# Kernel optimization log

Hardware: AMD Instinct MI355X
Metric: run time of the kernel (lower is better)

Reference implementation:

```python
import jax, jax.numpy as jnp
import numpy as np

CH_IN = 256
CH_OUT = 32


def setup_inputs() -> dict:
    key = jax.random.key(0)
    ks = jax.random.split(key, 7)
    b, c, H, W = 4, CH_IN, 64, 64
    x = jax.random.normal(ks[0], (b, c, H, W), dtype=jnp.float32)
    # 1x1 conv weights (out, in) and biases, small init like torch default
    sc_in = 1.0 / np.sqrt(CH_IN)
    Wf = jax.random.uniform(ks[1], (CH_OUT, CH_IN), jnp.float32, -sc_in, sc_in)
    bf = jax.random.uniform(ks[2], (CH_OUT,), jnp.float32, -sc_in, sc_in)
    Wg = jax.random.uniform(ks[3], (CH_OUT, CH_IN), jnp.float32, -sc_in, sc_in)
    bg = jax.random.uniform(ks[4], (CH_OUT,), jnp.float32, -sc_in, sc_in)
    Wh = jax.random.uniform(ks[5], (CH_IN, CH_IN), jnp.float32, -sc_in, sc_in)
    bh = jax.random.uniform(ks[6], (CH_IN,), jnp.float32, -sc_in, sc_in)
    return {"x": x, "Wf": Wf, "bf": bf, "Wg": Wg, "bg": bg, "Wh": Wh, "bh": bh}


def reference(x, Wf, bf, Wg, bg, Wh, bh):
    b, c, H, W = x.shape
    xf = x.reshape(b, c, H * W)                      # [b, c, N]
    # 1x1 convs == per-pixel linear projections
    f = jnp.einsum('oc,bcn->bon', Wf, xf) + bf[None, :, None]   # [b, ch_out, N]
    g = jnp.einsum('oc,bcn->bon', Wg, xf) + bg[None, :, None]   # [b, ch_out, N]
    h = jnp.einsum('oc,bcn->bon', Wh, xf) + bh[None, :, None]   # [b, ch_in, N]
    # s[b, i, j] = sum_o f[b,o,i] * g[b,o,j]
    s = jnp.einsum('boi,boj->bij', f, g)             # [b, N, N]
    # torch softmax over dim=1 (the i axis)
    beta = jax.nn.softmax(s, axis=1)                 # [b, N, N]
    # o = h @ beta : [b, c, N] x [b, N, N] -> [b, c, N]
    o = jnp.einsum('bcn,bnm->bcm', h, beta)
    return o.reshape(b, c, H, W)
```

## Files before the change

### kernel.cpp

```cpp
#include <hip/hip_runtime.h>
#include <hip/hip_bf16.h>
#include <math.h>

#define BATCH 4
#define CIN   256
#define DQK   32
#define NPIX  4096
#define MTOT  320

typedef __attribute__((ext_vector_type(4))) float f32x4;
typedef __attribute__((ext_vector_type(8))) short bf16x8;
typedef __attribute__((ext_vector_type(4))) unsigned int u32x4;

__device__ __forceinline__ unsigned short f2bf(float f) {
  unsigned u = __builtin_bit_cast(unsigned, f);
  u += 0x7FFFu + ((u >> 16) & 1u);
  return (unsigned short)(u >> 16);
}
__device__ __forceinline__ unsigned pk2(float a, float b) {
  return (unsigned)f2bf(a) | ((unsigned)f2bf(b) << 16);
}
__device__ __forceinline__ void wait_vm2_lgkm0() { asm volatile("s_waitcnt vmcnt(2) lgkmcnt(0)" ::: "memory"); }
__device__ __forceinline__ void wait_vm0_lgkm0() { asm volatile("s_waitcnt vmcnt(0) lgkmcnt(0)" ::: "memory"); }

#define GLD16(GP, LP) \
  __builtin_amdgcn_global_load_lds((const __attribute__((address_space(1))) void*)(GP), \
                                   (__attribute__((address_space(3))) void*)(LP), 16, 0, 0)

__global__ void wcvt(const float* __restrict__ Wh, const float* __restrict__ Wf,
                     const float* __restrict__ Wg,
                     const float* __restrict__ bh, const float* __restrict__ bf,
                     const float* __restrict__ bg,
                     unsigned short* __restrict__ Wb, float* __restrict__ bcat) {
  const int r = blockIdx.x;
  const int c = threadIdx.x;
  const float* src = (r < 256) ? &Wh[r * CIN] : (r < 288) ? &Wf[(r - 256) * CIN] : &Wg[(r - 288) * CIN];
  Wb[r * CIN + c] = f2bf(src[c]);
  if (c == 0)
    bcat[r] = (r < 256) ? bh[r] : (r < 288) ? bf[r - 256] : bg[r - 288];
}

#define XPAD 4
__launch_bounds__(512, 1)
__global__ void proj_all(const float* __restrict__ x, const unsigned short* __restrict__ Wb,
                         const float* __restrict__ bcat,
                         unsigned short* __restrict__ F, unsigned short* __restrict__ G,
                         unsigned short* __restrict__ H) {
  __shared__ unsigned short Xs[64 * (CIN + XPAD)];

  const int bid = blockIdx.x;
  const int b = bid >> 6;
  const int n0 = (bid & 63) << 6;
  const int t = threadIdx.x;
  const int lane = t & 63;
  const int w = t >> 6;

  const float* __restrict__ xb = x + (size_t)b * CIN * NPIX + n0;
#pragma unroll
  for (int p = 0; p < 16; ++p) {
    const int k = p * 16 + w * 2;
    const float a0 = xb[(size_t)k * NPIX + lane];
    const float a1 = xb[(size_t)(k + 1) * NPIX + lane];
    const unsigned pk = (unsigned)f2bf(a0) | ((unsigned)f2bf(a1) << 16);
    *(unsigned*)((char*)Xs + lane * (CIN + XPAD) * 2 + k * 2) = pk;
  }
  __syncthreads();

  const int l16 = lane & 15, lhi = lane >> 4;
  const int wm = w >> 1;
  const int wn = w & 1;

  const f32x4 fzero = {0.f, 0.f, 0.f, 0.f};
  f32x4 acc[5][2];
#pragma unroll
  for (int i = 0; i < 5; ++i)
#pragma unroll
    for (int j = 0; j < 2; ++j) acc[i][j] = fzero;

#pragma unroll
  for (int ks = 0; ks < 8; ++ks) {
    bf16x8 bx[2];
#pragma unroll
    for (int j = 0; j < 2; ++j)
      bx[j] = *(const bf16x8*)&Xs[(wn * 32 + j * 16 + l16) * (CIN + XPAD) + ks * 32 + lhi * 8];
#pragma unroll
    for (int i = 0; i < 5; ++i) {
      const bf16x8 aw = *(const bf16x8*)(Wb + (size_t)(wm * 80 + i * 16 + l16) * CIN + ks * 32 + lhi * 8);
#pragma unroll
      for (int j = 0; j < 2; ++j)
        acc[i][j] = __builtin_amdgcn_mfma_f32_16x16x32_bf16(aw, bx[j], acc[i][j], 0, 0, 0);
    }
  }

#pragma unroll
  for (int i = 0; i < 5; ++i) {
    const int MT = wm * 5 + i;
    const int m0 = MT * 16;
    const f32x4 bias = *(const f32x4*)&bcat[m0 + lhi * 4];
#pragma unroll
    for (int j = 0; j < 2; ++j) {
      const int n = n0 + wn * 32 + j * 16 + l16;
      f32x4 v = acc[i][j];
      v.x += bias.x; v.y += bias.y; v.z += bias.z; v.w += bias.w;
      if (MT < 16) {
        const int c0 = m0 + lhi * 4;
        unsigned short* dst = H + ((size_t)b * CIN + c0) * NPIX + n;
        dst[0 * NPIX] = f2bf(v.x);
        dst[1 * NPIX] = f2bf(v.y);
        dst[2 * NPIX] = f2bf(v.z);
        dst[3 * NPIX] = f2bf(v.w);
      } else {
        unsigned short* dst = (MT < 18) ? F : G;
        const int d0 = ((MT - 16) & 1) * 16 + lhi * 4;
        uint2 pk;
        pk.x = (unsigned)f2bf(v.x) | ((unsigned)f2bf(v.y) << 16);
        pk.y = (unsigned)f2bf(v.z) | ((unsigned)f2bf(v.w) << 16);
        *(uint2*)(dst + ((size_t)b * NPIX + n) * DQK + d0) = pk;
      }
    }
  }
}

#define BNK  64
#define KEYS 2048
#define NTILE (KEYS / BNK)

__launch_bounds__(1024, 1)
__global__ void attn_split(const unsigned short* __restrict__ F,
                           const unsigned short* __restrict__ G,
                           const unsigned short* __restrict__ H,
                           unsigned short* __restrict__ Ap, float* __restrict__ Lp) {
  __shared__ unsigned short Kl[3][64][32];
  __shared__ unsigned short Vl[3][256][64];
  __shared__ unsigned short Pl[2][4][32][72];

  const int bid = blockIdx.x;
  const int slab = bid & 7;
  const int b = slab >> 1;
  const int split = slab & 1;
  const int qt = bid >> 3;
  const int t = threadIdx.x;
  const int lane = t & 63, w = t >> 6;
  const int l16 = lane & 15, lhi = lane >> 4;
  const int mg = w >> 2, cs = w & 3;

  const unsigned short* Fb = F + (size_t)b * NPIX * DQK;
  const unsigned short* Gb = G + (size_t)b * NPIX * DQK;
  const unsigned short* Hb = H + (size_t)b * CIN * NPIX;
  const int nb0 = split * KEYS;
  const int q0 = qt * 128 + mg * 32;

  const f32x4 fzero = {0.f, 0.f, 0.f, 0.f};

  bf16x8 qf[2];
#pragma unroll
  for (int mt = 0; mt < 2; ++mt)
    qf[mt] = *(const bf16x8*)(Gb + (size_t)(q0 + mt * 16 + l16) * DQK + lhi * 8);

  f32x4 acc[4][2];
#pragma unroll
  for (int ct = 0; ct < 4; ++ct)
#pragma unroll
    for (int mt = 0; mt < 2; ++mt) acc[ct][mt] = fzero;
  float Lacc[2] = {0.f, 0.f};

  const char* vsrc = (const char*)Hb + ((size_t)(8 * w + (lane >> 3)) * NPIX + nb0) * 2
                   + (((lane & 7) ^ (lane >> 3)) * 16);
  const int kw = (w >= 12) ? (w - 12) : 0;
  const char* ksrc = (const char*)Fb + ((size_t)(nb0 + 16 * kw + (lane >> 2)) * DQK) * 2
                   + (((lane & 3) ^ ((lane >> 2) & 3)) * 16);

#define ISSUE(TT) do {                                                           \
    const int bu_ = (TT) % 3;                                                    \
    if (w >= 12)                                                                 \
      GLD16(ksrc + (size_t)(TT) * 64 * DQK * 2, &Kl[bu_][16 * kw][0]);           \
    _Pragma("unroll")                                                            \
    for (int i_ = 0; i_ < 2; ++i_)                                               \
      GLD16(vsrc + (size_t)i_ * 128 * NPIX * 2 + (size_t)(TT) * 128,             \
            &Vl[bu_][i_ * 128 + 8 * w][0]);                                      \
  } while (0)

#define QKSM(BUF3, PAR) do {                                                     \
    const unsigned short* kb_ = &Kl[BUF3][0][0];                                 \
    const bf16x8 kf_ = *(const bf16x8*)(kb_ + (cs * 16 + l16) * 32 + ((lhi ^ (l16 & 3)) * 8)); \
    f32x4 s_[2];                                                                 \
    _Pragma("unroll")                                                            \
    for (int mt_ = 0; mt_ < 2; ++mt_)                                            \
      s_[mt_] = __builtin_amdgcn_mfma_f32_16x16x32_bf16(kf_, qf[mt_], fzero, 0, 0, 0); \
    _Pragma("unroll")                                                            \
    for (int mt_ = 0; mt_ < 2; ++mt_) {                                          \
      const float p0 = __expf(s_[mt_][0]), p1 = __expf(s_[mt_][1]);              \
      const float p2 = __expf(s_[mt_][2]), p3 = __expf(s_[mt_][3]);              \
      Lacc[mt_] += (p0 + p1) + (p2 + p3);                                        \
      uint2 pk_; pk_.x = pk2(p0, p1); pk_.y = pk2(p2, p3);                       \
      *(uint2*)&Pl[PAR][mg][mt_ * 16 + l16][cs * 16 + lhi * 4] = pk_;            \
    }                                                                            \
  } while (0)

#define PVACC(BUF3, PF) do {                                                     \
    const unsigned short* vb_ = &Vl[BUF3][0][0];                                 \
    __builtin_amdgcn_s_setprio(1);                                               \
    _Pragma("unroll")                                                            \
    for (int kk_ = 0; kk_ < 2; ++kk_)                                            \
      _Pragma("unroll")                                                          \
      for (int ct_ = 0; ct_ < 4; ++ct_) {                                        \
        const bf16x8 vf_ = *(const bf16x8*)(vb_ + (cs * 64 + ct_ * 16 + l16) * 64 \
                            + (((4 * kk_ + lhi) ^ (l16 & 7)) * 8));              \
        _Pragma("unroll")                                                        \
        for (int mt_ = 0; mt_ < 2; ++mt_)                                        \
          acc[ct_][mt_] = __builtin_amdgcn_mfma_f32_16x16x32_bf16(vf_, PF[mt_][kk_], acc[ct_][mt_], 0, 0, 0); \
      }                                                                          \
    __builtin_amdgcn_s_setprio(0);                                               \
  } while (0)

  ISSUE(0); ISSUE(1);
  wait_vm2_lgkm0();
  __builtin_amdgcn_s_barrier();
  asm volatile("" ::: "memory");
  QKSM(0, 0);

  for (int tt = 0; tt < NTILE; ++tt) {
    const int par = tt & 1;
    if (tt == NTILE - 1) wait_vm0_lgkm0(); else wait_vm2_lgkm0();
    __builtin_amdgcn_s_barrier();
    asm volatile("" ::: "memory");
    if (tt + 2 < NTILE) ISSUE(tt + 2);
    bf16x8 pf[2][2];
#pragma unroll
    for (int mt = 0; mt < 2; ++mt)
#pragma unroll
      for (int kk = 0; kk < 2; ++kk)
        pf[mt][kk] = *(const bf16x8*)&Pl[par][mg][mt * 16 + l16][kk * 32 + lhi * 8];
    if (tt + 1 < NTILE) QKSM((tt + 1) % 3, par ^ 1);
    PVACC(tt % 3, pf);
  }
#undef ISSUE
#undef QKSM
#undef PVACC

#pragma unroll
  for (int mt = 0; mt < 2; ++mt) {
    float L = Lacc[mt];
    L += __shfl_xor(L, 16, 64);
    L += __shfl_xor(L, 32, 64);
    if (lhi == 0)
      Lp[((size_t)split * 4 + cs) * (4 * NPIX) + (size_t)b * NPIX + q0 + mt * 16 + l16] = L;
  }
#pragma unroll
  for (int ct = 0; ct < 4; ++ct)
#pragma unroll
    for (int mt = 0; mt < 2; ++mt) {
      const int c = cs * 64 + ct * 16 + lhi * 4;
      const int q = q0 + mt * 16 + l16;
      unsigned short* dst = Ap + (((size_t)split * 4 + b) * CIN + c) * NPIX + q;
#pragma unroll
      for (int v = 0; v < 4; ++v) dst[(size_t)v * NPIX] = f2bf(acc[ct][mt][v]);
    }
}

__global__ void combineL(const float* __restrict__ Lp, float* __restrict__ Linv) {
  const int idx = blockIdx.x * 256 + threadIdx.x;
  float s = 0.f;
#pragma unroll
  for (int i = 0; i < 8; ++i) s += Lp[(size_t)i * (4 * NPIX) + idx];
  Linv[idx] = 1.f / s;
}

__global__ void combine(const unsigned short* __restrict__ Ap, const float* __restrict__ Linv,
                        float* __restrict__ out) {
  const size_t base = ((size_t)blockIdx.x * 256 + threadIdx.x) * 8;
  const int b = (int)(base / ((size_t)CIN * NPIX));
  const int q = (int)(base % NPIX);
  const u32x4 a0 = *(const u32x4*)(Ap + base);
  const u32x4 a1 = *(const u32x4*)(Ap + (size_t)4 * CIN * NPIX + base);
  const float* lv = &Linv[(size_t)b * NPIX + q];
  float r[8];
#pragma unroll
  for (int i = 0; i < 4; ++i) {
    const float x0 = __builtin_bit_cast(float, (a0[i] & 0xFFFFu) << 16) +
                     __builtin_bit_cast(float, (a1[i] & 0xFFFFu) << 16);
    const float x1 = __builtin_bit_cast(float, (a0[i] & 0xFFFF0000u)) +
                     __builtin_bit_cast(float, (a1[i] & 0xFFFF0000u));
    r[2 * i] = x0 * lv[2 * i];
    r[2 * i + 1] = x1 * lv[2 * i + 1];
  }
  *(f32x4*)&out[base] = *(f32x4*)&r[0];
  *(f32x4*)&out[base + 4] = *(f32x4*)&r[4];
}

#define BN 32
__launch_bounds__(512, 2)
__global__ void attn_kernel(const unsigned short* __restrict__ F,
                            const unsigned short* __restrict__ G,
                            const unsigned short* __restrict__ H,
                            float* __restrict__ out) {
  __shared__ unsigned short Klds[32 * 40];
  __shared__ unsigned short Vlds[256 * 40];
  __shared__ unsigned short Plds[8][32 * 40];

  const int bid = blockIdx.x;
  const int b = bid >> 6;
  const int t = threadIdx.x;
  const int lane = t & 63;
  const int w = t >> 6;
  const int l16 = lane & 15;
  const int lhi = lane >> 4;
  const int m0 = ((bid & 63) << 6) + ((w >> 2) << 5);
  const int c0 = (w & 3) << 6;

  const f32x4 fzero = {0.f, 0.f, 0.f, 0.f};

  bf16x8 qf[2];
#pragma unroll
  for (int mt = 0; mt < 2; ++mt)
    qf[mt] = *(const bf16x8*)(G + ((size_t)b * NPIX + m0 + mt * 16 + l16) * DQK + lhi * 8);

  f32x4 acc[4][2];
#pragma unroll
  for (int ct = 0; ct < 4; ++ct)
#pragma unroll
    for (int mt = 0; mt < 2; ++mt) acc[ct][mt] = fzero;
  float Mr[2] = {-INFINITY, -INFINITY};
  float Lr[2] = {0.f, 0.f};

  const unsigned short* Fb = F + (size_t)b * NPIX * DQK;
  const unsigned short* Hb = H + (size_t)b * CIN * NPIX;
  unsigned short* Pw = &Plds[w][0];

  for (int n0 = 0; n0 < NPIX; n0 += BN) {
    __syncthreads();
    if (t < 128) {
      const int nr = t >> 2, sl = t & 3;
      *(u32x4*)&Klds[nr * 40 + sl * 8] = *(const u32x4*)(Fb + (size_t)(n0 + nr) * DQK + sl * 8);
    }
#pragma unroll
    for (int i = 0; i < 2; ++i) {
      const int q = t + i * 512;
      const int cr = q >> 2, sl = q & 3;
      *(u32x4*)&Vlds[cr * 40 + sl * 8] = *(const u32x4*)(Hb + (size_t)cr * NPIX + n0 + sl * 8);
    }
    __syncthreads();

    bf16x8 kf[2];
#pragma unroll
    for (int nts = 0; nts < 2; ++nts)
      kf[nts] = *(const bf16x8*)&Klds[(nts * 16 + l16) * 40 + lhi * 8];
    f32x4 s[2][2];
#pragma unroll
    for (int mt = 0; mt < 2; ++mt)
#pragma unroll
      for (int nts = 0; nts < 2; ++nts)
        s[mt][nts] = __builtin_amdgcn_mfma_f32_16x16x32_bf16(kf[nts], qf[mt], fzero, 0, 0, 0);

#pragma unroll
    for (int mt = 0; mt < 2; ++mt) {
      float tmax = s[mt][0][0];
#pragma unroll
      for (int v = 1; v < 4; ++v) tmax = fmaxf(tmax, s[mt][0][v]);
#pragma unroll
      for (int v = 0; v < 4; ++v) tmax = fmaxf(tmax, s[mt][1][v]);
      tmax = fmaxf(tmax, __shfl_xor(tmax, 16, 64));
      tmax = fmaxf(tmax, __shfl_xor(tmax, 32, 64));
      const float newM = fmaxf(Mr[mt], tmax);
      const float rescale = __expf(Mr[mt] - newM);
      Mr[mt] = newM;
      float p[2][4];
      float psum = 0.f;
#pragma unroll
      for (int nts = 0; nts < 2; ++nts)
#pragma unroll
        for (int v = 0; v < 4; ++v) {
          p[nts][v] = __expf(s[mt][nts][v] - newM);
          psum += p[nts][v];
        }
      psum += __shfl_xor(psum, 16, 64);
      psum += __shfl_xor(psum, 32, 64);
      Lr[mt] = Lr[mt] * rescale + psum;
#pragma unroll
      for (int ct = 0; ct < 4; ++ct) acc[ct][mt] *= rescale;
#pragma unroll
      for (int nts = 0; nts < 2; ++nts) {
        uint2 pkv;
        pkv.x = (unsigned)f2bf(p[nts][0]) | ((unsigned)f2bf(p[nts][1]) << 16);
        pkv.y = (unsigned)f2bf(p[nts][2]) | ((unsigned)f2bf(p[nts][3]) << 16);
        *(uint2*)&Pw[(mt * 16 + l16) * 40 + nts * 16 + lhi * 4] = pkv;
      }
    }
    asm volatile("" ::: "memory");

    bf16x8 pf[2];
#pragma unroll
    for (int mt = 0; mt < 2; ++mt)
      pf[mt] = *(const bf16x8*)&Pw[(mt * 16 + l16) * 40 + lhi * 8];
#pragma unroll
    for (int ct = 0; ct < 4; ++ct) {
      const bf16x8 vf = *(const bf16x8*)&Vlds[(c0 + ct * 16 + l16) * 40 + lhi * 8];
#pragma unroll
      for (int mt = 0; mt < 2; ++mt)
        acc[ct][mt] = __builtin_amdgcn_mfma_f32_16x16x32_bf16(vf, pf[mt], acc[ct][mt], 0, 0, 0);
    }
  }

#pragma unroll
  for (int mt = 0; mt < 2; ++mt) {
    const float invL = 1.f / Lr[mt];
    const int m = m0 + mt * 16 + l16;
#pragma unroll
    for (int ct = 0; ct < 4; ++ct)
#pragma unroll
      for (int v = 0; v < 4; ++v) {
        const int c = c0 + ct * 16 + lhi * 4 + v;
        out[((size_t)b * CIN + c) * NPIX + m] = acc[ct][mt][v] * invL;
      }
  }
}

extern "C" void kernel_launch(void* const* d_in, const int* in_sizes, int n_in,
                              void* d_out, int out_size, void* d_ws, size_t ws_size,
                              hipStream_t stream) {
  (void)in_sizes; (void)n_in; (void)out_size;
  const float* x  = (const float*)d_in[0];
  const float* Wf = (const float*)d_in[1];
  const float* bf = (const float*)d_in[2];
  const float* Wg = (const float*)d_in[3];
  const float* bg = (const float*)d_in[4];
  const float* Wh = (const float*)d_in[5];
  const float* bh = (const float*)d_in[6];
  float* out = (float*)d_out;

  unsigned short* Fw = (unsigned short*)d_ws;
  unsigned short* Gw = Fw + (size_t)BATCH * NPIX * DQK;
  unsigned short* Hw = Gw + (size_t)BATCH * NPIX * DQK;
  unsigned short* Wb = Hw + (size_t)BATCH * CIN * NPIX;
  float* bcat = (float*)(Wb + (size_t)MTOT * CIN);
  unsigned short* Apart = (unsigned short*)(bcat + MTOT);
  float* Lpart = (float*)(Apart + (size_t)2 * BATCH * CIN * NPIX);
  float* Linv  = Lpart + (size_t)8 * BATCH * NPIX;
  const size_t NEED = (size_t)((char*)(Linv + (size_t)BATCH * NPIX) - (char*)d_ws);

  hipLaunchKernelGGL(wcvt, dim3(MTOT), dim3(256), 0, stream, Wh, Wf, Wg, bh, bf, bg, Wb, bcat);
  hipLaunchKernelGGL(proj_all, dim3(BATCH * 64), dim3(512), 0, stream, x, Wb, bcat, Fw, Gw, Hw);

  if (ws_size >= NEED) {
    hipLaunchKernelGGL(attn_split, dim3(BATCH * 32 * 2), dim3(1024), 0, stream, Fw, Gw, Hw, Apart, Lpart);
    hipLaunchKernelGGL(combineL, dim3(BATCH * NPIX / 256), dim3(256), 0, stream, Lpart, Linv);
    hipLaunchKernelGGL(combine, dim3((size_t)BATCH * CIN * NPIX / 8 / 256), dim3(256), 0, stream, Apart, Linv, out);
  } else {
    hipLaunchKernelGGL(attn_kernel, dim3(BATCH * 64), dim3(512), 0, stream, Fw, Gw, Hw, out);
  }
}
```

Baseline: 81.71 us.

## Shrink attention blocks to 512 threads and 32-key tiles for two blocks per CU

The split attention kernel now uses 512-thread blocks covering 64 queries, with 32-key tiles instead of 64, and launches twice as many blocks. Two blocks can then share a CU under launch_bounds(512,2). The QK and softmax work is redistributed so each wave does one MFMA, and the row-sum partials drop from 8 to 4 per query. The aim is more resident waves and smaller LDS staging to hide latency, at the cost of more barriers per key and reloading K/V per smaller query tile, which doubles global V traffic.

```diff
diff --git a/kernel.cpp b/kernel.cpp
--- a/kernel.cpp
+++ b/kernel.cpp
@@ -121,18 +121,18 @@
   }
 }
 
-#define BNK  64
+#define BNK  32
 #define KEYS 2048
 #define NTILE (KEYS / BNK)
 
-__launch_bounds__(1024, 1)
+__launch_bounds__(512, 2)
 __global__ void attn_split(const unsigned short* __restrict__ F,
                            const unsigned short* __restrict__ G,
                            const unsigned short* __restrict__ H,
                            unsigned short* __restrict__ Ap, float* __restrict__ Lp) {
-  __shared__ unsigned short Kl[3][64][32];
-  __shared__ unsigned short Vl[3][256][64];
-  __shared__ unsigned short Pl[2][4][32][72];
+  __shared__ unsigned short Kl[3][32][32];
+  __shared__ unsigned short Vl[3][256][32];
+  __shared__ unsigned short Pl[2][2][32][40];
 
   const int bid = blockIdx.x;
   const int slab = bid & 7;
@@ -143,73 +143,67 @@
   const int lane = t & 63, w = t >> 6;
   const int l16 = lane & 15, lhi = lane >> 4;
   const int mg = w >> 2, cs = w & 3;
+  const int kt = cs & 1, mtq = cs >> 1;
 
   const unsigned short* Fb = F + (size_t)b * NPIX * DQK;
   const unsigned short* Gb = G + (size_t)b * NPIX * DQK;
   const unsigned short* Hb = H + (size_t)b * CIN * NPIX;
   const int nb0 = split * KEYS;
-  const int q0 = qt * 128 + mg * 32;
+  const int q0 = qt * 64 + mg * 32;
 
   const f32x4 fzero = {0.f, 0.f, 0.f, 0.f};
 
-  bf16x8 qf[2];
-#pragma unroll
-  for (int mt = 0; mt < 2; ++mt)
-    qf[mt] = *(const bf16x8*)(Gb + (size_t)(q0 + mt * 16 + l16) * DQK + lhi * 8);
+  const bf16x8 qf = *(const bf16x8*)(Gb + (size_t)(q0 + mtq * 16 + l16) * DQK + lhi * 8);
 
   f32x4 acc[4][2];
 #pragma unroll
   for (int ct = 0; ct < 4; ++ct)
 #pragma unroll
     for (int mt = 0; mt < 2; ++mt) acc[ct][mt] = fzero;
-  float Lacc[2] = {0.f, 0.f};
-
-  const char* vsrc = (const char*)Hb + ((size_t)(8 * w + (lane >> 3)) * NPIX + nb0) * 2
-                   + (((lane & 7) ^ (lane >> 3)) * 16);
-  const int kw = (w >= 12) ? (w - 12) : 0;
+  float Lacc = 0.f;
+
+  const char* vsrc = (const char*)Hb + ((size_t)(32 * w + (lane >> 2)) * NPIX + nb0) * 2
+                   + (((lane & 3) ^ ((lane >> 2) & 3)) * 16);
+  const int kw = (w == 5) ? 1 : 0;
   const char* ksrc = (const char*)Fb + ((size_t)(nb0 + 16 * kw + (lane >> 2)) * DQK) * 2
                    + (((lane & 3) ^ ((lane >> 2) & 3)) * 16);
 
 #define ISSUE(TT) do {                                                           \
     const int bu_ = (TT) % 3;                                                    \
-    if (w >= 12)                                                                 \
-      GLD16(ksrc + (size_t)(TT) * 64 * DQK * 2, &Kl[bu_][16 * kw][0]);           \
+    if (w == 4 || w == 5)                                                        \
+      GLD16(ksrc + (size_t)(TT) * 32 * DQK * 2, &Kl[bu_][16 * kw][0]);           \
     _Pragma("unroll")                                                            \
     for (int i_ = 0; i_ < 2; ++i_)                                               \
-      GLD16(vsrc + (size_t)i_ * 128 * NPIX * 2 + (size_t)(TT) * 128,             \
-            &Vl[bu_][i_ * 128 + 8 * w][0]);                                      \
+      GLD16(vsrc + (size_t)i_ * 16 * NPIX * 2 + (size_t)(TT) * BNK * 2,          \
+            &Vl[bu_][32 * w + 16 * i_][0]);                                      \
   } while (0)
 
 #define QKSM(BUF3, PAR) do {                                                     \
     const unsigned short* kb_ = &Kl[BUF3][0][0];                                 \
-    const bf16x8 kf_ = *(const bf16x8*)(kb_ + (cs * 16 + l16) * 32 + ((lhi ^ (l16 & 3)) * 8)); \
-    f32x4 s_[2];                                                                 \
+    const bf16x8 kf_ = *(const bf16x8*)(kb_ + (kt * 16 + l16) * 32 + ((lhi ^ (l16 & 3)) * 8)); \
+    const f32x4 s_ = __builtin_amdgcn_mfma_f32_16x16x32_bf16(kf_, qf, fzero, 0, 0, 0); \
+    const float p0 = __expf(s_[0]), p1 = __expf(s_[1]);                          \
+    const float p2 = __expf(s_[2]), p3 = __expf(s_[3]);                          \
+    Lacc += (p0 + p1) + (p2 + p3);                                               \
+    uint2 pk_; pk_.x = pk2(p0, p1); pk_.y = pk2(p2, p3);                         \
+    *(uint2*)&Pl[PAR][mg][mtq * 16 + l16][kt * 16 + lhi * 4] = pk_;              \
+  } while (0)
+
+#define PVACC(BUF3) do {                                                         \
+    const unsigned short* vb_ = &Vl[BUF3][0][0];                                 \
+    bf16x8 pf_[2];                                                               \
     _Pragma("unroll")                                                            \
     for (int mt_ = 0; mt_ < 2; ++mt_)                                            \
-      s_[mt_] = __builtin_amdgcn_mfma_f32_16x16x32_bf16(kf_, qf[mt_], fzero, 0, 0, 0); \
-    _Pragma("unroll")                                                            \
-    for (int mt_ = 0; mt_ < 2; ++mt_) {                                          \
-      const float p0 = __expf(s_[mt_][0]), p1 = __expf(s_[mt_][1]);              \
-      const float p2 = __expf(s_[mt_][2]), p3 = __expf(s_[mt_][3]);              \
-      Lacc[mt_] += (p0 + p1) + (p2 + p3);                                        \
-      uint2 pk_; pk_.x = pk2(p0, p1); pk_.y = pk2(p2, p3);                       \
-      *(uint2*)&Pl[PAR][mg][mt_ * 16 + l16][cs * 16 + lhi * 4] = pk_;            \
-    }                                                                            \
-  } while (0)
-
-#define PVACC(BUF3, PF) do {                                                     \
-    const unsigned short* vb_ = &Vl[BUF3][0][0];                                 \
+      pf_[mt_] = *(const bf16x8*)&Pl[par][mg][mt_ * 16 + l16][lhi * 8];          \
     __builtin_amdgcn_s_setprio(1);                                               \
     _Pragma("unroll")                                                            \
-    for (int kk_ = 0; kk_ < 2; ++kk_)                                            \
+    for (int ct_ = 0; ct_ < 4; ++ct_) {                                          \
+      const bf16x8 vf_ = *(const bf16x8*)(vb_ + (cs * 64 + ct_ * 16 + l16) * 32  \
+                          + ((lhi ^ (l16 & 3)) * 8));                            \
       _Pragma("unroll")                                                          \
-      for (int ct_ = 0; ct_ < 4; ++ct_) {                                        \
-        const bf16x8 vf_ = *(const bf16x8*)(vb_ + (cs * 64 + ct_ * 16 + l16) * 64 \
-                            + (((4 * kk_ + lhi) ^ (l16 & 7)) * 8));              \
-        _Pragma("unroll")                                                        \
-        for (int mt_ = 0; mt_ < 2; ++mt_)                                        \
-          acc[ct_][mt_] = __builtin_amdgcn_mfma_f32_16x16x32_bf16(vf_, PF[mt_][kk_], acc[ct_][mt_], 0, 0, 0); \
-      }                                                                          \
+      for (int mt_ = 0; mt_ < 2; ++mt_)                                          \
+        acc[ct_][mt_] = __builtin_amdgcn_mfma_f32_16x16x32_bf16(vf_, pf_[mt_], acc[ct_][mt_], 0, 0, 0); \
+    }                                                                            \
     __builtin_amdgcn_s_setprio(0);                                               \
   } while (0)
 
@@ -225,26 +219,19 @@
     __builtin_amdgcn_s_barrier();
     asm volatile("" ::: "memory");
     if (tt + 2 < NTILE) ISSUE(tt + 2);
-    bf16x8 pf[2][2];
-#pragma unroll
-    for (int mt = 0; mt < 2; ++mt)
-#pragma unroll
-      for (int kk = 0; kk < 2; ++kk)
-        pf[mt][kk] = *(const bf16x8*)&Pl[par][mg][mt * 16 + l16][kk * 32 + lhi * 8];
     if (tt + 1 < NTILE) QKSM((tt + 1) % 3, par ^ 1);
-    PVACC(tt % 3, pf);
+    PVACC(tt % 3);
   }
 #undef ISSUE
 #undef QKSM
 #undef PVACC
 
-#pragma unroll
-  for (int mt = 0; mt < 2; ++mt) {
-    float L = Lacc[mt];
+  {
+    float L = Lacc;
     L += __shfl_xor(L, 16, 64);
     L += __shfl_xor(L, 32, 64);
     if (lhi == 0)
-      Lp[((size_t)split * 4 + cs) * (4 * NPIX) + (size_t)b * NPIX + q0 + mt * 16 + l16] = L;
+      Lp[((size_t)split * 2 + kt) * (4 * NPIX) + (size_t)b * NPIX + q0 + mtq * 16 + l16] = L;
   }
 #pragma unroll
   for (int ct = 0; ct < 4; ++ct)
@@ -262,7 +249,7 @@
   const int idx = blockIdx.x * 256 + threadIdx.x;
   float s = 0.f;
 #pragma unroll
-  for (int i = 0; i < 8; ++i) s += Lp[(size_t)i * (4 * NPIX) + idx];
+  for (int i = 0; i < 4; ++i) s += Lp[(size_t)i * (4 * NPIX) + idx];
   Linv[idx] = 1.f / s;
 }
 
@@ -442,7 +429,7 @@
   hipLaunchKernelGGL(proj_all, dim3(BATCH * 64), dim3(512), 0, stream, x, Wb, bcat, Fw, Gw, Hw);
 
   if (ws_size >= NEED) {
-    hipLaunchKernelGGL(attn_split, dim3(BATCH * 32 * 2), dim3(1024), 0, stream, Fw, Gw, Hw, Apart, Lpart);
+    hipLaunchKernelGGL(attn_split, dim3(BATCH * 64 * 2), dim3(512), 0, stream, Fw, Gw, Hw, Apart, Lpart);
     hipLaunchKernelGGL(combineL, dim3(BATCH * NPIX / 256), dim3(256), 0, stream, Lpart, Linv);
     hipLaunchKernelGGL(combine, dim3((size_t)BATCH * CIN * NPIX / 8 / 256), dim3(256), 0, stream, Apart, Linv, out);
   } else {
```

Result: slower. 89.90 us (+10.0%).
